# Optimization experiments

Hardware: AMD Instinct MI355X
Metric: run time of the kernel (lower is better)

The kernel has to match this reference:

```python
import jax, jax.numpy as jnp
import numpy as np

KL_W, SIZ_W, DEN_W, MAT_W = 0.001, 0.05, 0.1, 0.1


def setup_inputs() -> dict:
    key = jax.random.key(0)
    ks = jax.random.split(key, 9)
    B, N, M, L = 4, 8192, 8192, 512
    return {
        "pred_pos": jax.random.normal(ks[0], (B, N, 3), jnp.float32),
        "pred_sizing": jax.random.normal(ks[1], (B, N, 1), jnp.float32),
        "pred_material": jax.random.normal(ks[2], (B, N, 4), jnp.float32),
        "target_pos": jax.random.normal(ks[3], (B, M, 3), jnp.float32),
        "target_sizing": jax.random.normal(ks[4], (B, N, 1), jnp.float32),
        "target_material": jax.random.normal(ks[5], (B, N, 4), jnp.float32),
        "mu": jax.random.normal(ks[6], (B, L), jnp.float32),
        "logvar": jax.random.normal(ks[7], (B, L), jnp.float32),
        "sub_idx": jax.random.randint(ks[8], (1024,), 0, N, jnp.int64),
    }


def _pairwise_sq(a, b):
    # squared euclidean distances: [B,N,M]
    a2 = jnp.sum(a * a, axis=-1)                     # [B,N]
    b2 = jnp.sum(b * b, axis=-1)                     # [B,M]
    ab = jnp.einsum('bnd,bmd->bnm', a, b)            # [B,N,M]
    return a2[:, :, None] + b2[:, None, :] - 2.0 * ab


def reference(pred_pos, pred_sizing, pred_material, target_pos,
              target_sizing, target_material, mu, logvar, sub_idx):
    # Chamfer: one pairwise matrix, min over both axes
    d = _pairwise_sq(pred_pos, target_pos)           # [B,N,M]
    cd = (jnp.min(d, axis=2).mean(axis=1) + jnp.min(d, axis=1).mean(axis=1)).mean()

    # KL divergence term
    kl = -0.5 * jnp.mean(1.0 + logvar - mu ** 2 - jnp.exp(logvar))

    # density uniformity on a 1024-point subsample
    pts = pred_pos[:, sub_idx]                       # [B,n,3]
    n = pts.shape[1]
    dd = _pairwise_sq(pts, pts) + jnp.eye(n, dtype=pts.dtype)[None] * 1e6
    nn_d = jnp.min(dd, axis=2)                       # [B,n]
    density = jnp.std(nn_d, axis=1, ddof=1).mean()   # torch .std is unbiased

    sizing_loss = jnp.mean((pred_sizing - target_sizing) ** 2)
    material_loss = jnp.mean((pred_material - target_material) ** 2)

    total = cd + KL_W * kl + DEN_W * density + SIZ_W * sizing_loss + MAT_W * material_loss
    return total
```

## Files before the change

### kernel.cpp

```cpp
#include <hip/hip_runtime.h>
#include <math.h>

#define BB 4
#define NN 8192
#define LL 512
#define NSUB 1024

#define AUX_BLOCKS 64
#define SL_BLOCKS 48
#define CH_BLOCKS 1024
#define PREP_BLOCKS 256

#define PPS_OFF 0
#define CHS_OFF 256
#define DNS_OFF 1280
#define KL_OFF  1312
#define SIZ_OFF 1360
#define MAT_OFF 1408
#define FRAG_OFF ((size_t)8192)
#define FRAG_SET ((size_t)BB * NN * 32)

typedef __bf16 bf16x8 __attribute__((ext_vector_type(8)));
typedef float f32x16 __attribute__((ext_vector_type(16)));

__device__ inline unsigned short f2bf(float f) {
    unsigned u = __float_as_uint(f);
    unsigned r = (u + 0x7FFFu + ((u >> 16) & 1u)) >> 16;
    return (unsigned short)r;
}
__device__ inline float bf2f(unsigned short h) {
    return __uint_as_float(((unsigned)h) << 16);
}
__device__ inline unsigned pk(unsigned short lo, unsigned short hi) {
    return (unsigned)lo | ((unsigned)hi << 16);
}

__device__ inline float blockReduceSum256(float v) {
    __shared__ float red[4];
    #pragma unroll
    for (int o = 32; o; o >>= 1) v += __shfl_down(v, o);
    __syncthreads();
    if ((threadIdx.x & 63) == 0) red[threadIdx.x >> 6] = v;
    __syncthreads();
    return red[0] + red[1] + red[2] + red[3];
}

__global__ __launch_bounds__(256) void prep_frags_kernel(
    const float* __restrict__ pred, const float* __restrict__ targ,
    unsigned char* __restrict__ frag, float* __restrict__ ws) {
    const int i = blockIdx.x * 256 + threadIdx.x;
    const int s = i >> 15;
    const int r = i & (BB * NN - 1);
    const int b = r >> 13;
    const int p = r & (NN - 1);
    const float* pos = (s ? targ : pred) + (size_t)r * 3;
    const float x = pos[0], y = pos[1], z = pos[2];
    const unsigned short hx = f2bf(x), hy = f2bf(y), hz = f2bf(z);
    const unsigned short lx = f2bf(x - bf2f(hx));
    const unsigned short ly = f2bf(y - bf2f(hy));
    const unsigned short lz = f2bf(z - bf2f(hz));
    const float pp = fmaf(x, x, fmaf(y, y, z * z));
    const float w = -0.5f * pp;
    const unsigned short wh = f2bf(w);
    const float wr = w - bf2f(wh);
    const unsigned short wl = f2bf(wr);
    const unsigned short wl2 = f2bf(wr - bf2f(wl));
    const unsigned short ONE = 0x3F80;

    uint4 a0, a1, b0, b1;
    a0.x = pk(hx, hy); a0.y = pk(hz, lx); a0.z = pk(ly, lz); a0.w = pk(hx, hy);
    a1.x = pk(hz, lx); a1.y = pk(ly, lz); a1.z = pk(ONE, ONE); a1.w = pk(ONE, 0);
    b0.x = pk(hx, hy); b0.y = pk(hz, hx); b0.z = pk(hy, hz); b0.w = pk(lx, ly);
    b1.x = pk(lz, lx); b1.y = pk(ly, lz); b1.z = pk(wh, wl); b1.w = pk(wl2, 0);

    uint4* Adst = (uint4*)(frag + (size_t)s * FRAG_SET) + (size_t)r * 2;
    Adst[0] = a0;
    Adst[1] = a1;
    uint4* Bdst = (uint4*)(frag + (2 + s) * FRAG_SET);
    const size_t bi = (size_t)b * NN * 2 + (size_t)(p >> 5) * 64 + (p & 31);
    Bdst[bi] = b0;
    Bdst[bi + 32] = b1;

    float sum = blockReduceSum256(pp);
    if (threadIdx.x == 0) ws[PPS_OFF + blockIdx.x] = sum;
}

__global__ __launch_bounds__(256, 4) void mega_kernel(
    const float* __restrict__ pred,
    const unsigned char* __restrict__ frag,
    const float* __restrict__ mu, const float* __restrict__ logvar,
    const float* __restrict__ psiz, const float* __restrict__ tsiz,
    const float* __restrict__ pmat, const float* __restrict__ tmat,
    const int* __restrict__ sub_idx, float* __restrict__ ws) {
    __shared__ __align__(16) unsigned char smem[16384];
    const int tid = threadIdx.x;
    const int bid = blockIdx.x;

    if (bid >= AUX_BLOCKS) {
        const int cid = bid - AUX_BLOCKS;
        const int rg = cid & 127;
        const int bd = cid >> 7;
        const int b = bd >> 1;
        const int dir = bd & 1;
        const int As = dir;
        const int Bs = dir ^ 1;
        const int w = tid >> 6, lane = tid & 63;
        const int lo5 = lane & 31, sel = lane >> 5;

        const uint4* Ap = (const uint4*)(frag + (size_t)As * FRAG_SET) +
                          (size_t)b * NN * 2;
        const int qbase = rg * 64;
        const bf16x8 A0 = __builtin_bit_cast(
            bf16x8, Ap[(size_t)(qbase + lo5) * 2 + sel]);
        const bf16x8 A1 = __builtin_bit_cast(
            bf16x8, Ap[(size_t)(qbase + 32 + lo5) * 2 + sel]);

        const uint4* Bp = (const uint4*)(frag + (size_t)(2 + Bs) * FRAG_SET) +
                          (size_t)b * NN * 2 + (size_t)w * 4096 + lane;

        f32x16 st0, st1;
        #pragma unroll
        for (int i = 0; i < 16; ++i) { st0[i] = -3e38f; st1[i] = -3e38f; }
        const f32x16 zc = {};

        uint4 c0 = Bp[0], c1 = Bp[64];
        #pragma unroll 1
        for (int it = 0; it < 32; ++it) {
            const uint4* nxt = Bp + (size_t)((it < 31 ? it + 1 : it) * 128);
            uint4 n0 = nxt[0];
            uint4 n1 = nxt[64];
            const bf16x8 B0 = __builtin_bit_cast(bf16x8, c0);
            const bf16x8 B1 = __builtin_bit_cast(bf16x8, c1);
            {
                f32x16 d0 = __builtin_amdgcn_mfma_f32_32x32x16_bf16(
                    A0, B0, zc, 0, 0, 0);
                f32x16 d1 = __builtin_amdgcn_mfma_f32_32x32x16_bf16(
                    A0, B1, zc, 0, 0, 0);
                #pragma unroll
                for (int i = 0; i < 16; ++i)
                    st0[i] = fmaxf(fmaxf(st0[i], d0[i]), d1[i]);
            }
            {
                f32x16 e0 = __builtin_amdgcn_mfma_f32_32x32x16_bf16(
                    A1, B0, zc, 0, 0, 0);
                f32x16 e1 = __builtin_amdgcn_mfma_f32_32x32x16_bf16(
                    A1, B1, zc, 0, 0, 0);
                #pragma unroll
                for (int i = 0; i < 16; ++i)
                    st1[i] = fmaxf(fmaxf(st1[i], e0[i]), e1[i]);
            }
            c0 = n0; c1 = n1;
        }

        #pragma unroll
        for (int m = 1; m <= 16; m <<= 1) {
            #pragma unroll
            for (int i = 0; i < 16; ++i) {
                st0[i] = fmaxf(st0[i], __shfl_xor(st0[i], m));
                st1[i] = fmaxf(st1[i], __shfl_xor(st1[i], m));
            }
        }
        float* sm = (float*)smem;
        if (lo5 == 0) {
            #pragma unroll
            for (int i = 0; i < 16; ++i) {
                const int r = (i & 3) + 8 * (i >> 2) + 4 * sel;
                sm[w * 64 + r] = st0[i];
                sm[w * 64 + 32 + r] = st1[i];
            }
        }
        __syncthreads();
        if (tid < 64) {
            float v = fmaxf(fmaxf(sm[tid], sm[64 + tid]),
                            fmaxf(sm[128 + tid], sm[192 + tid]));
            #pragma unroll
            for (int o = 32; o; o >>= 1) v += __shfl_down(v, o);
            if (tid == 0) ws[CHS_OFF + cid] = v;
        }
        return;
    }

    if (bid < 16) {
        float4* pts = (float4*)smem;
        const int chunk = bid & 3;
        const int b = bid >> 2;
        for (int k = tid; k < NSUB; k += 256) {
            int idx = sub_idx[k];
            const float* p = pred + ((size_t)b * NN + idx) * 3;
            float x = p[0], y = p[1], z = p[2];
            pts[k] = make_float4(x, y, z, -0.5f * fmaf(x, x, fmaf(y, y, z * z)));
        }
        __syncthreads();
        const int i = chunk * 256 + tid;
        const float4 me = pts[i];
        float h0 = -1e30f, h1 = -1e30f, h2 = -1e30f, h3 = -1e30f;
        #pragma unroll 4
        for (int j = 0; j < NSUB; j += 4) {
            float4 q0 = pts[j + 0], q1 = pts[j + 1], q2 = pts[j + 2], q3 = pts[j + 3];
            float t0 = fmaf(me.z, q0.z, q0.w);
            t0 = fmaf(me.y, q0.y, t0); t0 = fmaf(me.x, q0.x, t0);
            t0 = (j + 0 == i) ? -1e30f : t0; h0 = fmaxf(h0, t0);
            float t1 = fmaf(me.z, q1.z, q1.w);
            t1 = fmaf(me.y, q1.y, t1); t1 = fmaf(me.x, q1.x, t1);
            t1 = (j + 1 == i) ? -1e30f : t1; h1 = fmaxf(h1, t1);
            float t2 = fmaf(me.z, q2.z, q2.w);
            t2 = fmaf(me.y, q2.y, t2); t2 = fmaf(me.x, q2.x, t2);
            t2 = (j + 2 == i) ? -1e30f : t2; h2 = fmaxf(h2, t2);
            float t3 = fmaf(me.z, q3.z, q3.w);
            t3 = fmaf(me.y, q3.y, t3); t3 = fmaf(me.x, q3.x, t3);
            t3 = (j + 3 == i) ? -1e30f : t3; h3 = fmaxf(h3, t3);
        }
        float h = fmaxf(fmaxf(h0, h1), fmaxf(h2, h3));
        float pp = fmaf(me.x, me.x, fmaf(me.y, me.y, me.z * me.z));
        float m = pp - 2.0f * h;
        float s = blockReduceSum256(m); __syncthreads();
        float ss = blockReduceSum256(m * m);
        if (tid == 0) {
            ws[DNS_OFF + bid] = s;
            ws[DNS_OFF + 16 + bid] = ss;
        }
    } else {
        const int r = bid - 16;
        const int stride = SL_BLOCKS * 256;
        const int g0 = r * 256 + tid;
        float skl = 0.0f;
        for (int i = g0; i < BB * LL; i += stride) {
            float m = mu[i], lv = logvar[i];
            skl += 1.0f + lv - m * m - expf(lv);
        }
        float ssz = 0.0f;
        for (int i = g0; i < BB * NN; i += stride) {
            float d = psiz[i] - tsiz[i];
            ssz = fmaf(d, d, ssz);
        }
        float smt = 0.0f;
        for (int i = g0; i < BB * NN * 4; i += stride) {
            float d = pmat[i] - tmat[i];
            smt = fmaf(d, d, smt);
        }
        skl = blockReduceSum256(skl); __syncthreads();
        ssz = blockReduceSum256(ssz); __syncthreads();
        smt = blockReduceSum256(smt);
        if (tid == 0) {
            ws[KL_OFF + r] = skl;
            ws[SIZ_OFF + r] = ssz;
            ws[MAT_OFF + r] = smt;
        }
    }
}

__global__ __launch_bounds__(256) void finalize_kernel(
    const float* __restrict__ ws, float* __restrict__ out) {
    const int t = threadIdx.x;
    float pp = ws[PPS_OFF + t];
    float ch = ws[CHS_OFF + t] + ws[CHS_OFF + 256 + t] +
               ws[CHS_OFF + 512 + t] + ws[CHS_OFF + 768 + t];
    float kl = (t < SL_BLOCKS) ? ws[KL_OFF + t] : 0.0f;
    float sz = (t < SL_BLOCKS) ? ws[SIZ_OFF + t] : 0.0f;
    float mt = (t < SL_BLOCKS) ? ws[MAT_OFF + t] : 0.0f;
    float s_pp = blockReduceSum256(pp); __syncthreads();
    float s_ch = blockReduceSum256(ch); __syncthreads();
    float s_kl = blockReduceSum256(kl); __syncthreads();
    float s_sz = blockReduceSum256(sz); __syncthreads();
    float s_mt = blockReduceSum256(mt);
    if (t == 0) {
        float den = 0.0f;
        #pragma unroll
        for (int b = 0; b < BB; ++b) {
            float s = ws[DNS_OFF + 4 * b + 0] + ws[DNS_OFF + 4 * b + 1] +
                      ws[DNS_OFF + 4 * b + 2] + ws[DNS_OFF + 4 * b + 3];
            float q = ws[DNS_OFF + 16 + 4 * b + 0] + ws[DNS_OFF + 16 + 4 * b + 1] +
                      ws[DNS_OFF + 16 + 4 * b + 2] + ws[DNS_OFF + 16 + 4 * b + 3];
            float var = (q - s * s / (float)NSUB) / (float)(NSUB - 1);
            den += sqrtf(fmaxf(var, 0.0f));
        }
        den *= (1.0f / BB);
        float cd = (s_pp - 2.0f * s_ch) / (float)(BB * NN);
        float klv = -0.5f * s_kl / (float)(BB * LL);
        float sizing = s_sz / (float)(BB * NN);
        float material = s_mt / (float)(BB * NN * 4);
        out[0] = cd + 0.001f * klv + 0.1f * den + 0.05f * sizing +
                 0.1f * material;
    }
}

extern "C" void kernel_launch(void* const* d_in, const int* in_sizes, int n_in,
                              void* d_out, int out_size, void* d_ws,
                              size_t ws_size, hipStream_t stream) {
    const float* pred_pos = (const float*)d_in[0];
    const float* pred_siz = (const float*)d_in[1];
    const float* pred_mat = (const float*)d_in[2];
    const float* targ_pos = (const float*)d_in[3];
    const float* targ_siz = (const float*)d_in[4];
    const float* targ_mat = (const float*)d_in[5];
    const float* mu = (const float*)d_in[6];
    const float* logvar = (const float*)d_in[7];
    const int* sub_idx = (const int*)d_in[8];
    float* out = (float*)d_out;
    float* ws = (float*)d_ws;
    unsigned char* frag = (unsigned char*)d_ws + FRAG_OFF;

    prep_frags_kernel<<<PREP_BLOCKS, 256, 0, stream>>>(pred_pos, targ_pos,
                                                       frag, ws);
    mega_kernel<<<AUX_BLOCKS + CH_BLOCKS, 256, 0, stream>>>(
        pred_pos, frag, mu, logvar, pred_siz, targ_siz, pred_mat, targ_mat,
        sub_idx, ws);
    finalize_kernel<<<1, 256, 0, stream>>>(ws, out);
}
```

Measured before the change: 41.76 us.

## Fuse finalize into mega kernel via atomic ticket and deepen B prefetch

Measured after the change: 69.26 us. 1.66x slower.

```diff
diff --git a/kernel.cpp b/kernel.cpp
--- a/kernel.cpp
+++ b/kernel.cpp
@@ -9,14 +9,11 @@
 #define AUX_BLOCKS 64
 #define SL_BLOCKS 48
 #define CH_BLOCKS 1024
+#define TOT_BLOCKS (AUX_BLOCKS + CH_BLOCKS)
 #define PREP_BLOCKS 256
 
-#define PPS_OFF 0
-#define CHS_OFF 256
-#define DNS_OFF 1280
-#define KL_OFF  1312
-#define SIZ_OFF 1360
-#define MAT_OFF 1408
+#define TICKET 12
+#define PPS_OFF 16
 #define FRAG_OFF ((size_t)8192)
 #define FRAG_SET ((size_t)BB * NN * 32)
 
@@ -48,6 +45,8 @@
 __global__ __launch_bounds__(256) void prep_frags_kernel(
     const float* __restrict__ pred, const float* __restrict__ targ,
     unsigned char* __restrict__ frag, float* __restrict__ ws) {
+    if (blockIdx.x == 0 && threadIdx.x < 16) ws[threadIdx.x] = 0.0f;
+
     const int i = blockIdx.x * 256 + threadIdx.x;
     const int s = i >> 15;
     const int r = i & (BB * NN - 1);
@@ -91,7 +90,8 @@
     const float* __restrict__ mu, const float* __restrict__ logvar,
     const float* __restrict__ psiz, const float* __restrict__ tsiz,
     const float* __restrict__ pmat, const float* __restrict__ tmat,
-    const int* __restrict__ sub_idx, float* __restrict__ ws) {
+    const int* __restrict__ sub_idx, float* __restrict__ ws,
+    float* __restrict__ out) {
     __shared__ __align__(16) unsigned char smem[16384];
     const int tid = threadIdx.x;
     const int bid = blockIdx.x;
@@ -115,20 +115,26 @@
         const bf16x8 A1 = __builtin_bit_cast(
             bf16x8, Ap[(size_t)(qbase + 32 + lo5) * 2 + sel]);
 
-        const uint4* Bp = (const uint4*)(frag + (size_t)(2 + Bs) * FRAG_SET) +
-                          (size_t)b * NN * 2 + (size_t)w * 4096 + lane;
+        const uint4* Bit = (const uint4*)(frag + (size_t)(2 + Bs) * FRAG_SET) +
+                           (size_t)b * NN * 2 + (size_t)w * 4096 + lane;
+
+        float z0 = 0.0f;
+        asm("" : "+v"(z0));
+        f32x16 zc;
+        #pragma unroll
+        for (int i = 0; i < 16; ++i) zc[i] = z0;
 
         f32x16 st0, st1;
         #pragma unroll
         for (int i = 0; i < 16; ++i) { st0[i] = -3e38f; st1[i] = -3e38f; }
-        const f32x16 zc = {};
-
-        uint4 c0 = Bp[0], c1 = Bp[64];
+
+        uint4 c0 = Bit[0], c1 = Bit[64];
+        uint4 n0 = Bit[128], n1 = Bit[192];
         #pragma unroll 1
         for (int it = 0; it < 32; ++it) {
-            const uint4* nxt = Bp + (size_t)((it < 31 ? it + 1 : it) * 128);
-            uint4 n0 = nxt[0];
-            uint4 n1 = nxt[64];
+            const uint4* pf = Bit + ((it < 30) ? 256 : 0);
+            uint4 m0 = pf[0];
+            uint4 m1 = pf[64];
             const bf16x8 B0 = __builtin_bit_cast(bf16x8, c0);
             const bf16x8 B1 = __builtin_bit_cast(bf16x8, c1);
             {
@@ -150,6 +156,8 @@
                     st1[i] = fmaxf(fmaxf(st1[i], e0[i]), e1[i]);
             }
             c0 = n0; c1 = n1;
+            n0 = m0; n1 = m1;
+            Bit += 128;
         }
 
         #pragma unroll
@@ -175,12 +183,9 @@
                             fmaxf(sm[128 + tid], sm[192 + tid]));
             #pragma unroll
             for (int o = 32; o; o >>= 1) v += __shfl_down(v, o);
-            if (tid == 0) ws[CHS_OFF + cid] = v;
-        }
-        return;
-    }
-
-    if (bid < 16) {
+            if (tid == 0) atomicAdd(&ws[0], v);
+        }
+    } else if (bid < 16) {
         float4* pts = (float4*)smem;
         const int chunk = bid & 3;
         const int b = bid >> 2;
@@ -216,8 +221,8 @@
         float s = blockReduceSum256(m); __syncthreads();
         float ss = blockReduceSum256(m * m);
         if (tid == 0) {
-            ws[DNS_OFF + bid] = s;
-            ws[DNS_OFF + 16 + bid] = ss;
+            atomicAdd(&ws[4 + b], s);
+            atomicAdd(&ws[8 + b], ss);
         }
     } else {
         const int r = bid - 16;
@@ -242,45 +247,42 @@
         ssz = blockReduceSum256(ssz); __syncthreads();
         smt = blockReduceSum256(smt);
         if (tid == 0) {
-            ws[KL_OFF + r] = skl;
-            ws[SIZ_OFF + r] = ssz;
-            ws[MAT_OFF + r] = smt;
+            atomicAdd(&ws[1], skl);
+            atomicAdd(&ws[2], ssz);
+            atomicAdd(&ws[3], smt);
         }
     }
-}
-
-__global__ __launch_bounds__(256) void finalize_kernel(
-    const float* __restrict__ ws, float* __restrict__ out) {
-    const int t = threadIdx.x;
-    float pp = ws[PPS_OFF + t];
-    float ch = ws[CHS_OFF + t] + ws[CHS_OFF + 256 + t] +
-               ws[CHS_OFF + 512 + t] + ws[CHS_OFF + 768 + t];
-    float kl = (t < SL_BLOCKS) ? ws[KL_OFF + t] : 0.0f;
-    float sz = (t < SL_BLOCKS) ? ws[SIZ_OFF + t] : 0.0f;
-    float mt = (t < SL_BLOCKS) ? ws[MAT_OFF + t] : 0.0f;
-    float s_pp = blockReduceSum256(pp); __syncthreads();
-    float s_ch = blockReduceSum256(ch); __syncthreads();
-    float s_kl = blockReduceSum256(kl); __syncthreads();
-    float s_sz = blockReduceSum256(sz); __syncthreads();
-    float s_mt = blockReduceSum256(mt);
-    if (t == 0) {
-        float den = 0.0f;
-        #pragma unroll
-        for (int b = 0; b < BB; ++b) {
-            float s = ws[DNS_OFF + 4 * b + 0] + ws[DNS_OFF + 4 * b + 1] +
-                      ws[DNS_OFF + 4 * b + 2] + ws[DNS_OFF + 4 * b + 3];
-            float q = ws[DNS_OFF + 16 + 4 * b + 0] + ws[DNS_OFF + 16 + 4 * b + 1] +
-                      ws[DNS_OFF + 16 + 4 * b + 2] + ws[DNS_OFF + 16 + 4 * b + 3];
-            float var = (q - s * s / (float)NSUB) / (float)(NSUB - 1);
-            den += sqrtf(fmaxf(var, 0.0f));
-        }
-        den *= (1.0f / BB);
-        float cd = (s_pp - 2.0f * s_ch) / (float)(BB * NN);
-        float klv = -0.5f * s_kl / (float)(BB * LL);
-        float sizing = s_sz / (float)(BB * NN);
-        float material = s_mt / (float)(BB * NN * 4);
-        out[0] = cd + 0.001f * klv + 0.1f * den + 0.05f * sizing +
-                 0.1f * material;
+
+    __syncthreads();
+    int* flag = (int*)smem;
+    if (tid == 0) {
+        __threadfence();
+        unsigned t = atomicAdd((unsigned*)&ws[TICKET], 1u);
+        *flag = (t == TOT_BLOCKS - 1) ? 1 : 0;
+    }
+    __syncthreads();
+    if (*flag) {
+        float pp = ws[PPS_OFF + tid];
+        float s_pp = blockReduceSum256(pp);
+        if (tid == 0) {
+            float a[12];
+            #pragma unroll
+            for (int i = 0; i < 12; ++i) a[i] = atomicAdd(&ws[i], 0.0f);
+            float den = 0.0f;
+            #pragma unroll
+            for (int b = 0; b < BB; ++b) {
+                float sm = a[4 + b], qq = a[8 + b];
+                float var = (qq - sm * sm / (float)NSUB) / (float)(NSUB - 1);
+                den += sqrtf(fmaxf(var, 0.0f));
+            }
+            den *= (1.0f / BB);
+            float cd = (s_pp - 2.0f * a[0]) / (float)(BB * NN);
+            float klv = -0.5f * a[1] / (float)(BB * LL);
+            float sizing = a[2] / (float)(BB * NN);
+            float material = a[3] / (float)(BB * NN * 4);
+            out[0] = cd + 0.001f * klv + 0.1f * den + 0.05f * sizing +
+                     0.1f * material;
+        }
     }
 }
 
@@ -302,8 +304,7 @@
 
     prep_frags_kernel<<<PREP_BLOCKS, 256, 0, stream>>>(pred_pos, targ_pos,
                                                        frag, ws);
-    mega_kernel<<<AUX_BLOCKS + CH_BLOCKS, 256, 0, stream>>>(
+    mega_kernel<<<TOT_BLOCKS, 256, 0, stream>>>(
         pred_pos, frag, mu, logvar, pred_siz, targ_siz, pred_mat, targ_mat,
-        sub_idx, ws);
-    finalize_kernel<<<1, 256, 0, stream>>>(ws, out);
-}
+        sub_idx, ws, out);
+}
```
